# Kernel optimization log

Measured on AMD Instinct MI355X. Metric: run time of the kernel, lower is better.

The kernel has to match this reference:

```python
import jax, jax.numpy as jnp
import numpy as np

MAX_NUM_POINTS = 2048
MAX_NUM_PERSONS = 8
CHUNK = 1024  # matches torch chunk_size


def setup_inputs() -> dict:
    key = jax.random.key(0)
    k1, k2 = jax.random.split(key)
    shape = (4, 3, (MAX_NUM_POINTS + 1) * MAX_NUM_PERSONS)
    return {
        "predictions": jax.random.normal(k1, shape, dtype=jnp.float32),
        "targets": jax.random.normal(k2, shape, dtype=jnp.float32),
    }


def _one_direction(a, b):
    # a, b: [B, N, 3]; for each point in a, min euclidean distance to b, summed over N.
    B, N, _ = a.shape
    b_sq = jnp.sum(b * b, axis=-1)  # [B, N]
    chunks = a.reshape(B, N // CHUNK, CHUNK, 3).transpose(1, 0, 2, 3)  # [n_chunks, B, C, 3]

    def step(carry, chunk):  # chunk: [B, C, 3]
        a_sq = jnp.sum(chunk * chunk, axis=-1)  # [B, C]
        d2 = a_sq[:, :, None] + b_sq[:, None, :] - 2.0 * jnp.einsum('bcd,bnd->bcn', chunk, b)
        d = jnp.sqrt(jnp.maximum(d2, 0.0))  # [B, C, N]
        return carry + jnp.sum(jnp.min(d, axis=2), axis=1), None

    total, _ = jax.lax.scan(step, jnp.zeros((B,), a.dtype), chunks)
    return total / N  # [B]


def _chamfer(pred, tgt):
    # pred, tgt: [B, N, 3]
    return jnp.mean((_one_direction(pred, tgt) + _one_direction(tgt, pred)) * 0.5)


def reference(predictions, targets):
    B = predictions.shape[0]
    P, K = MAX_NUM_POINTS, MAX_NUM_PERSONS
    x = predictions.reshape(B, 3, K, P + 1)
    y = targets.reshape(B, 3, K, P + 1)

    pred_indicator = x[:, 0, :, P]  # [B, K] logits
    target_indicator = (y[:, 0, :, P] > 0.5).astype(jnp.float32)  # [B, K]

    # BCEWithLogitsLoss, mean reduction (numerically stable form)
    z, t = pred_indicator, target_indicator
    detection_loss = jnp.mean(jnp.maximum(z, 0.0) - z * t + jnp.log1p(jnp.exp(-jnp.abs(z))))

    # clouds: [B, 3, K, P] -> [B, K*P, 3] (point order irrelevant for chamfer)
    pred_cloud = x[:, :, :, :P].transpose(0, 2, 3, 1).reshape(B, K * P, 3)
    target_cloud = y[:, :, :, :P].transpose(0, 2, 3, 1).reshape(B, K * P, 3)

    point_cloud_loss = _chamfer(pred_cloud, target_cloud)
    return detection_loss + point_cloud_loss
```

## Files before the change

### kernel.cpp

```cpp
#include <hip/hip_runtime.h>
#include <math.h>

#define PP 2048
#define KK 8
#define BB 4
#define NN 16384
#define CSTRIDE 16392
#define BSTRIDE 49176

#define FRAGS 4
#define ROWS_PER_BLOCK 512
#define ROWBLOCKS 32
#define NSLICES 8
#define SLICEPTS 2048
#define CHUNKPTS 512
#define TILES 16

typedef _Float16 f16;
typedef __attribute__((ext_vector_type(8))) _Float16 f16x8;
typedef __attribute__((ext_vector_type(16))) float f32x16;

__device__ __forceinline__ float min3f(float a, float b, float c) {
    return fminf(fminf(a, b), c);
}

__global__ __launch_bounds__(256) void init_min_kernel(unsigned* __restrict__ mins) {
    int i = blockIdx.x * 256 + threadIdx.x;
    mins[i] = 0x7F7FFFFFu;
}

__global__ __launch_bounds__(256, 4) void chamfer_mfma_kernel(
        const float* __restrict__ Apts, const float* __restrict__ Bpts,
        unsigned* __restrict__ minOut) {
    __shared__ f16x8 karr[2 * CHUNKPTS];

    const int tid  = threadIdx.x;
    const int lane = tid & 63;
    const int wave = tid >> 6;
    const int col  = lane & 31;
    const int g2   = lane >> 5;
    const int b     = blockIdx.z;
    const int slice = blockIdx.y;
    const int rowblock = blockIdx.x;

    f16x8 bop[FRAGS];
    float asq[FRAGS], acc[FRAGS];
    const int rbase = rowblock * ROWS_PER_BLOCK + wave * (FRAGS * 32);
#pragma unroll
    for (int f = 0; f < FRAGS; ++f) {
        int r = rbase + f * 32 + col;
        int abase = b * BSTRIDE + (r >> 11) * (PP + 1) + (r & (PP - 1));
        float ax = Apts[abase];
        float ay = Apts[abase + CSTRIDE];
        float az = Apts[abase + 2 * CSTRIDE];
        asq[f] = fmaf(ax, ax, fmaf(ay, ay, az * az));
        acc[f] = 1.0e30f;
        f16 h0 = (f16)ax, h1 = (f16)ay, h2 = (f16)az;
        f16 l0 = (f16)(ax - (float)h0);
        f16 l1 = (f16)(ay - (float)h1);
        f16 l2 = (f16)(az - (float)h2);
        f16x8 v;
#pragma unroll
        for (int j = 0; j < 8; ++j) v[j] = (f16)0.f;
        if (g2 == 0) {
            v[0] = -h0; v[1] = -h1; v[2] = -h2;
            v[3] = -h0; v[4] = -h1; v[5] = -h2;
            v[6] = -l0; v[7] = -l1;
        } else {
            v[0] = -l2; v[1] = (f16)1.f; v[2] = (f16)1.f;
        }
        bop[f] = v;
    }

    f32x16 Z16;
#pragma unroll
    for (int j = 0; j < 16; ++j) Z16[j] = 0.f;

    const int planebase = b * BSTRIDE + slice * (PP + 1);

    for (int c = 0; c < SLICEPTS / CHUNKPTS; ++c) {
        __syncthreads();
#pragma unroll
        for (int q = 0; q < 2; ++q) {
            int p  = tid + q * 256;
            int gb = planebase + c * CHUNKPTS + p;
            float x = Bpts[gb];
            float y = Bpts[gb + CSTRIDE];
            float z = Bpts[gb + 2 * CSTRIDE];
            f16 h0 = (f16)x, h1 = (f16)y, h2 = (f16)z;
            f16 l0 = (f16)(x - (float)h0);
            f16 l1 = (f16)(y - (float)h1);
            f16 l2 = (f16)(z - (float)h2);
            float bsq = 0.5f * fmaf(x, x, fmaf(y, y, z * z));
            f16 sh = (f16)bsq;
            f16 sl = (f16)(bsq - (float)sh);
            f16x8 lo;
            lo[0] = h0; lo[1] = h1; lo[2] = h2;
            lo[3] = l0; lo[4] = l1; lo[5] = l2;
            lo[6] = h0; lo[7] = h1;
            f16x8 hi;
#pragma unroll
            for (int j = 0; j < 8; ++j) hi[j] = (f16)0.f;
            hi[0] = h2; hi[1] = sh; hi[2] = sl;
            karr[p] = lo;
            karr[CHUNKPTS + p] = hi;
        }
        __syncthreads();

        const f16x8* kptr = karr + g2 * CHUNKPTS + col;
#pragma unroll 2
        for (int t = 0; t < TILES; ++t) {
            f16x8 af = kptr[t * 32];
#pragma unroll
            for (int f = 0; f < FRAGS; ++f) {
                f32x16 d = __builtin_amdgcn_mfma_f32_32x32x16_f16(af, bop[f], Z16, 0, 0, 0);
                float m0 = min3f(d[0],  d[1],  d[2]);
                float m1 = min3f(d[3],  d[4],  d[5]);
                float m2 = min3f(d[6],  d[7],  d[8]);
                float m3 = min3f(d[9],  d[10], d[11]);
                float m4 = min3f(d[12], d[13], d[14]);
                float n0 = min3f(m0, m1, m2);
                float n1 = min3f(m3, m4, d[15]);
                acc[f] = min3f(acc[f], n0, n1);
            }
        }
    }

#pragma unroll
    for (int f = 0; f < FRAGS; ++f) {
        float m = acc[f];
        m = fminf(m, __shfl_xor(m, 32));
        if (lane < 32) {
            float d2 = fmaxf(fmaf(2.0f, m, asq[f]), 0.0f);
            atomicMin(&minOut[b * NN + rbase + f * 32 + col], __float_as_uint(d2));
        }
    }
}

__global__ __launch_bounds__(256) void partial_reduce_kernel(
        const unsigned* __restrict__ mins, float* __restrict__ partials) {
    int tid = threadIdx.x;
    float s = 0.f;
    for (int i = blockIdx.x * 256 + tid; i < 2 * BB * NN; i += 128 * 256) {
        s += sqrtf(__uint_as_float(mins[i]));
    }
    __shared__ float red[256];
    red[tid] = s;
    __syncthreads();
    for (int off = 128; off > 0; off >>= 1) {
        if (tid < off) red[tid] += red[tid + off];
        __syncthreads();
    }
    if (tid == 0) partials[blockIdx.x] = red[0];
}

__global__ __launch_bounds__(128) void final_kernel(
        const float* __restrict__ partials,
        const float* __restrict__ pred, const float* __restrict__ tgt,
        float* __restrict__ out) {
    int tid = threadIdx.x;
    float v = partials[tid] * (1.0f / 131072.0f);
    if (tid < 32) {
        int b = tid >> 3, k = tid & 7;
        int idx = b * BSTRIDE + k * (PP + 1) + PP;
        float z = pred[idx];
        float t = tgt[idx] > 0.5f ? 1.0f : 0.0f;
        v += (fmaxf(z, 0.f) - z * t + log1pf(expf(-fabsf(z)))) * (1.0f / 32.0f);
    }
    __shared__ float red[128];
    red[tid] = v;
    __syncthreads();
    for (int off = 64; off > 0; off >>= 1) {
        if (tid < off) red[tid] += red[tid + off];
        __syncthreads();
    }
    if (tid == 0) out[0] = red[0];
}

extern "C" void kernel_launch(void* const* d_in, const int* in_sizes, int n_in,
                              void* d_out, int out_size, void* d_ws, size_t ws_size,
                              hipStream_t stream) {
    const float* pred = (const float*)d_in[0];
    const float* tgt  = (const float*)d_in[1];
    float* out = (float*)d_out;

    unsigned* mins = (unsigned*)d_ws;
    float* partials = (float*)((char*)d_ws + 2 * BB * NN * sizeof(unsigned));

    init_min_kernel<<<2 * BB * NN / 256, 256, 0, stream>>>(mins);
    dim3 grid(ROWBLOCKS, NSLICES, BB);
    chamfer_mfma_kernel<<<grid, 256, 0, stream>>>(pred, tgt, mins);
    chamfer_mfma_kernel<<<grid, 256, 0, stream>>>(tgt, pred, mins + BB * NN);
    partial_reduce_kernel<<<128, 256, 0, stream>>>(mins, partials);
    final_kernel<<<1, 128, 0, stream>>>(partials, pred, tgt, out);
}
```

Measured before the change: 76.32 us.

## Merge both chamfer directions into one launch, enlarge tiles, fuse reductions

Both chamfer directions now run in a single kernel launch, with the direction chosen from blockIdx.z. Each block covers 1024 rows using 8 fragments per wave and sweeps 4096 points across 4 slices, so operand reuse per block goes up and the number of atomicMin collisions goes down. The two final reduction kernels become one 1024-thread single-block kernel, cutting total launches from five to three. The costs are higher register pressure (launch bounds lowered to 2 blocks per CU), a grid that shrinks from 1024 to 512 blocks, and a serial single-block reduction over 131k values.

```diff
diff --git a/kernel.cpp b/kernel.cpp
--- a/kernel.cpp
+++ b/kernel.cpp
@@ -8,11 +8,11 @@
 #define CSTRIDE 16392
 #define BSTRIDE 49176
 
-#define FRAGS 4
-#define ROWS_PER_BLOCK 512
-#define ROWBLOCKS 32
-#define NSLICES 8
-#define SLICEPTS 2048
+#define FRAGS 8
+#define ROWS_PER_BLOCK 1024
+#define ROWBLOCKS 16
+#define NSLICES 4
+#define SLICEPTS 4096
 #define CHUNKPTS 512
 #define TILES 16
 
@@ -29,9 +29,9 @@
     mins[i] = 0x7F7FFFFFu;
 }
 
-__global__ __launch_bounds__(256, 4) void chamfer_mfma_kernel(
-        const float* __restrict__ Apts, const float* __restrict__ Bpts,
-        unsigned* __restrict__ minOut) {
+__global__ __launch_bounds__(256, 2) void chamfer_mfma_kernel(
+        const float* __restrict__ pred, const float* __restrict__ tgt,
+        unsigned* __restrict__ mins) {
     __shared__ f16x8 karr[2 * CHUNKPTS];
 
     const int tid  = threadIdx.x;
@@ -39,9 +39,14 @@
     const int wave = tid >> 6;
     const int col  = lane & 31;
     const int g2   = lane >> 5;
-    const int b     = blockIdx.z;
+    const int dir  = blockIdx.z >> 2;
+    const int b    = blockIdx.z & 3;
     const int slice = blockIdx.y;
     const int rowblock = blockIdx.x;
+
+    const float* __restrict__ Apts = dir ? tgt : pred;
+    const float* __restrict__ Bpts = dir ? pred : tgt;
+    unsigned* __restrict__ minOut = mins + dir * BB * NN;
 
     f16x8 bop[FRAGS];
     float asq[FRAGS], acc[FRAGS];
@@ -76,14 +81,13 @@
 #pragma unroll
     for (int j = 0; j < 16; ++j) Z16[j] = 0.f;
 
-    const int planebase = b * BSTRIDE + slice * (PP + 1);
-
     for (int c = 0; c < SLICEPTS / CHUNKPTS; ++c) {
         __syncthreads();
 #pragma unroll
         for (int q = 0; q < 2; ++q) {
             int p  = tid + q * 256;
-            int gb = planebase + c * CHUNKPTS + p;
+            int cj = slice * SLICEPTS + c * CHUNKPTS + p;
+            int gb = b * BSTRIDE + (cj >> 11) * (PP + 1) + (cj & (PP - 1));
             float x = Bpts[gb];
             float y = Bpts[gb + CSTRIDE];
             float z = Bpts[gb + 2 * CSTRIDE];
@@ -108,7 +112,6 @@
         __syncthreads();
 
         const f16x8* kptr = karr + g2 * CHUNKPTS + col;
-#pragma unroll 2
         for (int t = 0; t < TILES; ++t) {
             f16x8 af = kptr[t * 32];
 #pragma unroll
@@ -137,29 +140,16 @@
     }
 }
 
-__global__ __launch_bounds__(256) void partial_reduce_kernel(
-        const unsigned* __restrict__ mins, float* __restrict__ partials) {
-    int tid = threadIdx.x;
-    float s = 0.f;
-    for (int i = blockIdx.x * 256 + tid; i < 2 * BB * NN; i += 128 * 256) {
-        s += sqrtf(__uint_as_float(mins[i]));
-    }
-    __shared__ float red[256];
-    red[tid] = s;
-    __syncthreads();
-    for (int off = 128; off > 0; off >>= 1) {
-        if (tid < off) red[tid] += red[tid + off];
-        __syncthreads();
-    }
-    if (tid == 0) partials[blockIdx.x] = red[0];
-}
-
-__global__ __launch_bounds__(128) void final_kernel(
-        const float* __restrict__ partials,
+__global__ __launch_bounds__(1024) void reduce_final_kernel(
+        const unsigned* __restrict__ mins,
         const float* __restrict__ pred, const float* __restrict__ tgt,
         float* __restrict__ out) {
     int tid = threadIdx.x;
-    float v = partials[tid] * (1.0f / 131072.0f);
+    float s = 0.f;
+    for (int i = tid; i < 2 * BB * NN; i += 1024) {
+        s += sqrtf(__uint_as_float(mins[i]));
+    }
+    float v = s * (1.0f / 131072.0f);
     if (tid < 32) {
         int b = tid >> 3, k = tid & 7;
         int idx = b * BSTRIDE + k * (PP + 1) + PP;
@@ -167,10 +157,10 @@
         float t = tgt[idx] > 0.5f ? 1.0f : 0.0f;
         v += (fmaxf(z, 0.f) - z * t + log1pf(expf(-fabsf(z)))) * (1.0f / 32.0f);
     }
-    __shared__ float red[128];
+    __shared__ float red[1024];
     red[tid] = v;
     __syncthreads();
-    for (int off = 64; off > 0; off >>= 1) {
+    for (int off = 512; off > 0; off >>= 1) {
         if (tid < off) red[tid] += red[tid + off];
         __syncthreads();
     }
@@ -185,12 +175,9 @@
     float* out = (float*)d_out;
 
     unsigned* mins = (unsigned*)d_ws;
-    float* partials = (float*)((char*)d_ws + 2 * BB * NN * sizeof(unsigned));
 
     init_min_kernel<<<2 * BB * NN / 256, 256, 0, stream>>>(mins);
-    dim3 grid(ROWBLOCKS, NSLICES, BB);
+    dim3 grid(ROWBLOCKS, NSLICES, 2 * BB);
     chamfer_mfma_kernel<<<grid, 256, 0, stream>>>(pred, tgt, mins);
-    chamfer_mfma_kernel<<<grid, 256, 0, stream>>>(tgt, pred, mins + BB * NN);
-    partial_reduce_kernel<<<128, 256, 0, stream>>>(mins, partials);
-    final_kernel<<<1, 128, 0, stream>>>(partials, pred, tgt, out);
+    reduce_final_kernel<<<1, 1024, 0, stream>>>(mins, pred, tgt, out);
 }
```

Result: slower. 117.1 us (+53.4%).
